# Optimization experiments

Measured on AMD Instinct MI355X. Metric: run time of the kernel, lower is better.

Reference implementation:

```python
import jax, jax.numpy as jnp
import numpy as np

NUM_HEADS = 8
H_NUM, W_NUM = 1, 2   # idx=0 stripe windows
SCALE = float((256 // NUM_HEADS) ** -0.5)  # qk_scale


def _partition(x, h_sp, w_sp):
    # x: (T,B,C,H,W) -> (T, B*nWin, heads, N, C//heads) with N = h_sp*w_sp
    T, B, C, H, W = x.shape
    x = x.reshape(T, B, C, H // h_sp, h_sp, W // w_sp, w_sp)
    x = x.transpose(0, 1, 3, 5, 4, 6, 2)  # T,B,nH,nW,h_sp,w_sp,C
    x = x.reshape(T, -1, h_sp * w_sp, NUM_HEADS, C // NUM_HEADS)
    return x.transpose(0, 1, 3, 2, 4)


def setup_inputs() -> dict:
    key = jax.random.key(0)
    k1, k2, k3 = jax.random.split(key, 3)
    shape = (4, 2, 256, 56, 56)
    return {
        "q": jax.random.normal(k1, shape, jnp.float32),
        "k": jax.random.normal(k2, shape, jnp.float32),
        "v": jax.random.normal(k3, shape, jnp.float32),
        "v_lamda": 1,
    }


def reference(q, k, v, v_lamda):
    T, B, C, H0, W0 = q.shape
    h_pad = (-H0) % H_NUM
    w_pad = (-W0) % W_NUM
    pad = ((0, 0), (0, 0), (0, 0), (0, h_pad), (0, w_pad))
    q = jnp.pad(q, pad)
    k = jnp.pad(k, pad)
    v = jnp.pad(v, pad)
    H, W = H0 + h_pad, W0 + w_pad
    h_sp, w_sp = H // H_NUM, W // W_NUM

    qw = _partition(q, h_sp, w_sp)  # (T, BnW, h, N, d)
    kw = _partition(k, h_sp, w_sp)
    vw = _partition(v, h_sp, w_sp)  # head dim = C*v_lamda//heads

    attn = jnp.einsum('twhnd,twhmd->twhnm', qw, kw)          # (QK^T), no softmax
    out = jnp.einsum('twhnm,twhmd->twhnd', attn, vw) * (SCALE * 2)

    # merge windows back: (T,BnW,h,N,d) -> (T,B,Cv,H,W)
    Cv = C * v_lamda
    out = out.transpose(0, 1, 3, 2, 4).reshape(T, -1, h_sp * w_sp, Cv)
    out = out.reshape(T, B, H_NUM, W_NUM, h_sp, w_sp, Cv)
    out = out.transpose(0, 1, 2, 4, 3, 5, 6).reshape(T, B, H, W, Cv)
    out = out.transpose(0, 1, 4, 2, 3)
    return out[:, :, :, :H0, :W0]
```

## Files before the change

kernel.cpp:

```cpp
#include <hip/hip_runtime.h>


#define HW 3136
#define WDIM 56
#define NPROB 128
#define SPLIT 14
#define PSPLIT 112
#define SCALE2 0.35355339059327373f

typedef const __attribute__((address_space(1))) void gas_void;
typedef __attribute__((address_space(3))) void las_void;
typedef float v2f __attribute__((ext_vector_type(2)));

__global__ __launch_bounds__(256) void kv_kernel(const float* __restrict__ K,
                                                 const float* __restrict__ V,
                                                 float* __restrict__ Mpart) {
    __shared__ float lds[2 * 32 * PSPLIT];

    const int blk = blockIdx.x;
    const int p   = blk / SPLIT;
    const int s   = blk - p * SPLIT;
    const int head = p & 7;
    const int win  = (p >> 3) & 1;
    const int b    = (p >> 4) & 1;
    const int t    = p >> 5;

    const size_t base = (size_t)((t * 2 + b) * 256 + head * 32) * HW;
    const float* __restrict__ Kb = K + base;
    const float* __restrict__ Vb = V + base;

    const int tid = threadIdx.x;
    const int l   = tid & 63;
    const int w   = tid >> 6;

    #pragma unroll
    for (int i = 0; i < 7; ++i) {
        const int q    = (w * 7 + i) * 64 + l;
        const int isv  = q >= 896 ? 1 : 0;
        const int r    = q - isv * 896;
        const int pq   = r >> 5;
        const int slot = r & 31;
        const int ch   = ((slot & 7) << 2) + (slot >> 3);
        const int n    = s * PSPLIT + pq * 4;
        const int y    = n / 28;
        const int x    = n - y * 28;
        const float* src = (isv ? Vb : Kb)
                         + (size_t)ch * HW + y * WDIM + win * 28 + x;
        float* dst = &lds[(w * 7 + i) * 256];
        __builtin_amdgcn_global_load_lds((gas_void*)src, (las_void*)dst, 16, 0, 0);
    }
    __syncthreads();

    const int g = l >> 3;
    const int e = l & 7;

    v2f acc2[4][4] = {};
    #pragma unroll
    for (int j = 0; j < 7; ++j) {
        const int rowb = (7 * w + j) * 128;
        float4 ka[4], va[4];
        #pragma unroll
        for (int i = 0; i < 4; ++i) {
            ka[i] = *(const float4*)&lds[rowb + (g + 8 * i) * 4];
            va[i] = *(const float4*)&lds[3584 + rowb + (e + 8 * i) * 4];
        }
        #pragma unroll
        for (int i = 0; i < 4; ++i) {
            const v2f ka_lo = {ka[i].x, ka[i].y};
            const v2f ka_hi = {ka[i].z, ka[i].w};
            #pragma unroll
            for (int jj = 0; jj < 4; ++jj) {
                const v2f va_lo = {va[jj].x, va[jj].y};
                const v2f va_hi = {va[jj].z, va[jj].w};
                acc2[i][jj] += ka_lo * va_lo;
                acc2[i][jj] += ka_hi * va_hi;
            }
        }
    }
    __syncthreads();

    const int dd0 = g * 4;
    const int de0 = e * 4;
    #pragma unroll
    for (int i = 0; i < 4; ++i)
        #pragma unroll
        for (int jj = 0; jj < 4; ++jj)
            lds[w * 1024 + (dd0 + i) * 32 + (de0 + jj)] = acc2[i][jj].x + acc2[i][jj].y;
    __syncthreads();

    const float4 r0 = *(const float4*)&lds[tid * 4];
    const float4 r1 = *(const float4*)&lds[1024 + tid * 4];
    const float4 r2 = *(const float4*)&lds[2048 + tid * 4];
    const float4 r3 = *(const float4*)&lds[3072 + tid * 4];
    float4 o;
    o.x = r0.x + r1.x + r2.x + r3.x;
    o.y = r0.y + r1.y + r2.y + r3.y;
    o.z = r0.z + r1.z + r2.z + r3.z;
    o.w = r0.w + r1.w + r2.w + r3.w;
    *(float4*)&Mpart[(size_t)blk * 1024 + tid * 4] = o;
}

__global__ __launch_bounds__(256) void qm_kernel(const float* __restrict__ Q,
                                                 const float* __restrict__ Mpart,
                                                 float* __restrict__ Out) {
    __shared__ float M[1024];
    const int blk = blockIdx.x;
    const int p   = blk / 7;
    const int c   = blk - p * 7;
    const int tid = threadIdx.x;

    const float* mp = Mpart + (size_t)p * SPLIT * 1024 + tid * 4;
    v2f s0 = {0.f, 0.f}, s1 = {0.f, 0.f};
    #pragma unroll
    for (int s = 0; s < SPLIT; ++s) {
        const float4 v = *(const float4*)&mp[s * 1024];
        const v2f vlo = {v.x, v.y};
        const v2f vhi = {v.z, v.w};
        s0 += vlo; s1 += vhi;
    }
    float4 sum;
    sum.x = s0.x * SCALE2; sum.y = s0.y * SCALE2;
    sum.z = s1.x * SCALE2; sum.w = s1.y * SCALE2;
    *(float4*)&M[tid * 4] = sum;
    __syncthreads();

    const int head = p & 7;
    const int win  = (p >> 3) & 1;
    const int b    = (p >> 4) & 1;
    const int t    = p >> 5;

    if (tid < 224) {
        const int n = c * 224 + tid;
        const int y = n / 28;
        const int x = n - y * 28;
        const size_t base = (size_t)((t * 2 + b) * 256 + head * 32) * HW
                          + y * WDIM + win * 28 + x;
        const float* __restrict__ Qb = Q + base;
        float* __restrict__ Ob = Out + base;

        float qv[32];
        #pragma unroll
        for (int dd = 0; dd < 32; ++dd)
            qv[dd] = Qb[(size_t)dd * HW];

        v2f acc2[16] = {};
        #pragma unroll 8
        for (int dd = 0; dd < 32; ++dd) {
            const v2f qq = {qv[dd], qv[dd]};
            #pragma unroll
            for (int gg = 0; gg < 8; ++gg) {
                const float4 m = *(const float4*)&M[dd * 32 + gg * 4];
                const v2f mlo = {m.x, m.y};
                const v2f mhi = {m.z, m.w};
                acc2[gg * 2 + 0] += qq * mlo;
                acc2[gg * 2 + 1] += qq * mhi;
            }
        }
        #pragma unroll
        for (int gg = 0; gg < 8; ++gg) {
            Ob[(size_t)(gg * 4 + 0) * HW] = acc2[gg * 2 + 0].x;
            Ob[(size_t)(gg * 4 + 1) * HW] = acc2[gg * 2 + 0].y;
            Ob[(size_t)(gg * 4 + 2) * HW] = acc2[gg * 2 + 1].x;
            Ob[(size_t)(gg * 4 + 3) * HW] = acc2[gg * 2 + 1].y;
        }
    }
}

extern "C" void kernel_launch(void* const* d_in, const int* in_sizes, int n_in,
                              void* d_out, int out_size, void* d_ws, size_t ws_size,
                              hipStream_t stream) {
    const float* q = (const float*)d_in[0];
    const float* k = (const float*)d_in[1];
    const float* v = (const float*)d_in[2];
    float* out   = (float*)d_out;
    float* Mpart = (float*)d_ws;

    kv_kernel<<<NPROB * SPLIT, 256, 0, stream>>>(k, v, Mpart);
    qm_kernel<<<NPROB * 7, 256, 0, stream>>>(q, Mpart, out);
}
```

Baseline: 129.2 us.

## Double-buffer KV reduction over fewer blocks and vectorize Q·M per-thread tiles

The KV kernel now runs 256 blocks that each loop over seven chunks with double-buffered global-to-LDS loads, explicit vmcnt waits and barriers, instead of 1792 single-chunk blocks. This cuts the partial-sum count from 14 to 2 per problem and lightens the Mpart reduction in the QM kernel. The QM kernel now gives each thread four pixels with float4 Q loads and float4 output stores, also over 256 blocks. The cost is much less parallelism: 256 blocks on a large GPU may leave CUs idle, and the wider accumulator set raises register pressure.

```diff
diff --git a/kernel.cpp b/kernel.cpp
--- a/kernel.cpp
+++ b/kernel.cpp
@@ -4,7 +4,6 @@
 #define HW 3136
 #define WDIM 56
 #define NPROB 128
-#define SPLIT 14
 #define PSPLIT 112
 #define SCALE2 0.35355339059327373f
 
@@ -15,11 +14,13 @@
 __global__ __launch_bounds__(256) void kv_kernel(const float* __restrict__ K,
                                                  const float* __restrict__ V,
                                                  float* __restrict__ Mpart) {
-    __shared__ float lds[2 * 32 * PSPLIT];
+    __shared__ float lds[2 * 7168];
+    float* bufA = lds;
+    float* bufB = lds + 7168;
 
-    const int blk = blockIdx.x;
-    const int p   = blk / SPLIT;
-    const int s   = blk - p * SPLIT;
+    const int g = blockIdx.x;
+    const int p = g >> 1;
+    const int h = g & 1;
     const int head = p & 7;
     const int win  = (p >> 3) & 1;
     const int b    = (p >> 4) & 1;
@@ -33,6 +34,7 @@
     const int l   = tid & 63;
     const int w   = tid >> 6;
 
+    const float* srcs[7];
     #pragma unroll
     for (int i = 0; i < 7; ++i) {
         const int q    = (w * 7 + i) * 64 + l;
@@ -41,45 +43,67 @@
         const int pq   = r >> 5;
         const int slot = r & 31;
         const int ch   = ((slot & 7) << 2) + (slot >> 3);
-        const int n    = s * PSPLIT + pq * 4;
+        const int n    = h * 7 * PSPLIT + pq * 4;
         const int y    = n / 28;
         const int x    = n - y * 28;
-        const float* src = (isv ? Vb : Kb)
-                         + (size_t)ch * HW + y * WDIM + win * 28 + x;
-        float* dst = &lds[(w * 7 + i) * 256];
-        __builtin_amdgcn_global_load_lds((gas_void*)src, (las_void*)dst, 16, 0, 0);
+        srcs[i] = (isv ? Vb : Kb) + (size_t)ch * HW + y * WDIM + win * 28 + x;
     }
-    __syncthreads();
 
-    const int g = l >> 3;
-    const int e = l & 7;
+    auto stage = [&](int c, float* buf) {
+        #pragma unroll
+        for (int i = 0; i < 7; ++i)
+            __builtin_amdgcn_global_load_lds((gas_void*)(srcs[i] + c * 224),
+                                             (las_void*)&buf[(w * 7 + i) * 256],
+                                             16, 0, 0);
+    };
 
+    const int gg = l >> 3;
+    const int e  = l & 7;
     v2f acc2[4][4] = {};
-    #pragma unroll
-    for (int j = 0; j < 7; ++j) {
-        const int rowb = (7 * w + j) * 128;
-        float4 ka[4], va[4];
+
+    auto compute = [&](const float* __restrict__ buf) {
         #pragma unroll
-        for (int i = 0; i < 4; ++i) {
-            ka[i] = *(const float4*)&lds[rowb + (g + 8 * i) * 4];
-            va[i] = *(const float4*)&lds[3584 + rowb + (e + 8 * i) * 4];
-        }
-        #pragma unroll
-        for (int i = 0; i < 4; ++i) {
-            const v2f ka_lo = {ka[i].x, ka[i].y};
-            const v2f ka_hi = {ka[i].z, ka[i].w};
+        for (int j = 0; j < 7; ++j) {
+            const int rowb = (7 * w + j) * 128;
+            float4 ka[4], va[4];
             #pragma unroll
-            for (int jj = 0; jj < 4; ++jj) {
-                const v2f va_lo = {va[jj].x, va[jj].y};
-                const v2f va_hi = {va[jj].z, va[jj].w};
-                acc2[i][jj] += ka_lo * va_lo;
-                acc2[i][jj] += ka_hi * va_hi;
+            for (int i = 0; i < 4; ++i) {
+                ka[i] = *(const float4*)&buf[rowb + (gg + 8 * i) * 4];
+                va[i] = *(const float4*)&buf[3584 + rowb + (e + 8 * i) * 4];
+            }
+            #pragma unroll
+            for (int i = 0; i < 4; ++i) {
+                const v2f ka_lo = {ka[i].x, ka[i].y};
+                const v2f ka_hi = {ka[i].z, ka[i].w};
+                #pragma unroll
+                for (int jj = 0; jj < 4; ++jj) {
+                    const v2f va_lo = {va[jj].x, va[jj].y};
+                    const v2f va_hi = {va[jj].z, va[jj].w};
+                    acc2[i][jj] += ka_lo * va_lo;
+                    acc2[i][jj] += ka_hi * va_hi;
+                }
             }
         }
+    };
+
+    stage(0, bufA);
+    stage(1, bufB);
+    #pragma unroll
+    for (int c = 0; c < 7; ++c) {
+        __builtin_amdgcn_sched_barrier(0);
+        if (c < 6) asm volatile("s_waitcnt vmcnt(7)" ::: "memory");
+        else       asm volatile("s_waitcnt vmcnt(0)" ::: "memory");
+        __builtin_amdgcn_sched_barrier(0);
+        __builtin_amdgcn_s_barrier();
+        __builtin_amdgcn_sched_barrier(0);
+        compute((c & 1) ? bufB : bufA);
+        __builtin_amdgcn_sched_barrier(0);
+        __builtin_amdgcn_s_barrier();
+        __builtin_amdgcn_sched_barrier(0);
+        if (c + 2 <= 6) stage(c + 2, (c & 1) ? bufB : bufA);
     }
-    __syncthreads();
 
-    const int dd0 = g * 4;
+    const int dd0 = gg * 4;
     const int de0 = e * 4;
     #pragma unroll
     for (int i = 0; i < 4; ++i)
@@ -97,30 +121,26 @@
     o.y = r0.y + r1.y + r2.y + r3.y;
     o.z = r0.z + r1.z + r2.z + r3.z;
     o.w = r0.w + r1.w + r2.w + r3.w;
-    *(float4*)&Mpart[(size_t)blk * 1024 + tid * 4] = o;
+    *(float4*)&Mpart[(size_t)g * 1024 + tid * 4] = o;
 }
 
 __global__ __launch_bounds__(256) void qm_kernel(const float* __restrict__ Q,
                                                  const float* __restrict__ Mpart,
                                                  float* __restrict__ Out) {
     __shared__ float M[1024];
-    const int blk = blockIdx.x;
-    const int p   = blk / 7;
-    const int c   = blk - p * 7;
+    const int g = blockIdx.x;
+    const int p = g >> 1;
+    const int h = g & 1;
     const int tid = threadIdx.x;
 
-    const float* mp = Mpart + (size_t)p * SPLIT * 1024 + tid * 4;
-    v2f s0 = {0.f, 0.f}, s1 = {0.f, 0.f};
-    #pragma unroll
-    for (int s = 0; s < SPLIT; ++s) {
-        const float4 v = *(const float4*)&mp[s * 1024];
-        const v2f vlo = {v.x, v.y};
-        const v2f vhi = {v.z, v.w};
-        s0 += vlo; s1 += vhi;
-    }
+    const float* mp = Mpart + (size_t)p * 2048 + tid * 4;
+    const float4 a0 = *(const float4*)mp;
+    const float4 a1 = *(const float4*)(mp + 1024);
     float4 sum;
-    sum.x = s0.x * SCALE2; sum.y = s0.y * SCALE2;
-    sum.z = s1.x * SCALE2; sum.w = s1.y * SCALE2;
+    sum.x = (a0.x + a1.x) * SCALE2;
+    sum.y = (a0.y + a1.y) * SCALE2;
+    sum.z = (a0.z + a1.z) * SCALE2;
+    sum.w = (a0.w + a1.w) * SCALE2;
     *(float4*)&M[tid * 4] = sum;
     __syncthreads();
 
@@ -129,39 +149,37 @@
     const int b    = (p >> 4) & 1;
     const int t    = p >> 5;
 
-    if (tid < 224) {
-        const int n = c * 224 + tid;
-        const int y = n / 28;
-        const int x = n - y * 28;
+    if (tid < 196) {
+        const int qd = h * 196 + tid;
+        const int y  = qd / 7;
+        const int x  = (qd - y * 7) * 4;
         const size_t base = (size_t)((t * 2 + b) * 256 + head * 32) * HW
                           + y * WDIM + win * 28 + x;
         const float* __restrict__ Qb = Q + base;
         float* __restrict__ Ob = Out + base;
 
-        float qv[32];
-        #pragma unroll
-        for (int dd = 0; dd < 32; ++dd)
-            qv[dd] = Qb[(size_t)dd * HW];
-
-        v2f acc2[16] = {};
+        v2f accL[32] = {};
+        v2f accH[32] = {};
         #pragma unroll 8
         for (int dd = 0; dd < 32; ++dd) {
-            const v2f qq = {qv[dd], qv[dd]};
+            const float4 q4 = *(const float4*)&Qb[(size_t)dd * HW];
+            const v2f qL = {q4.x, q4.y};
+            const v2f qH = {q4.z, q4.w};
             #pragma unroll
-            for (int gg = 0; gg < 8; ++gg) {
-                const float4 m = *(const float4*)&M[dd * 32 + gg * 4];
-                const v2f mlo = {m.x, m.y};
-                const v2f mhi = {m.z, m.w};
-                acc2[gg * 2 + 0] += qq * mlo;
-                acc2[gg * 2 + 1] += qq * mhi;
+            for (int de4 = 0; de4 < 8; ++de4) {
+                const float4 m = *(const float4*)&M[dd * 32 + de4 * 4];
+                accL[de4 * 4 + 0] += qL * m.x;  accH[de4 * 4 + 0] += qH * m.x;
+                accL[de4 * 4 + 1] += qL * m.y;  accH[de4 * 4 + 1] += qH * m.y;
+                accL[de4 * 4 + 2] += qL * m.z;  accH[de4 * 4 + 2] += qH * m.z;
+                accL[de4 * 4 + 3] += qL * m.w;  accH[de4 * 4 + 3] += qH * m.w;
             }
         }
         #pragma unroll
-        for (int gg = 0; gg < 8; ++gg) {
-            Ob[(size_t)(gg * 4 + 0) * HW] = acc2[gg * 2 + 0].x;
-            Ob[(size_t)(gg * 4 + 1) * HW] = acc2[gg * 2 + 0].y;
-            Ob[(size_t)(gg * 4 + 2) * HW] = acc2[gg * 2 + 1].x;
-            Ob[(size_t)(gg * 4 + 3) * HW] = acc2[gg * 2 + 1].y;
+        for (int de = 0; de < 32; ++de) {
+            float4 o;
+            o.x = accL[de].x; o.y = accL[de].y;
+            o.z = accH[de].x; o.w = accH[de].y;
+            *(float4*)&Ob[(size_t)de * HW] = o;
         }
     }
 }
@@ -175,6 +193,6 @@
     float* out   = (float*)d_out;
     float* Mpart = (float*)d_ws;
 
-    kv_kernel<<<NPROB * SPLIT, 256, 0, stream>>>(k, v, Mpart);
-    qm_kernel<<<NPROB * 7, 256, 0, stream>>>(q, Mpart, out);
+    kv_kernel<<<256, 256, 0, stream>>>(k, v, Mpart);
+    qm_kernel<<<256, 256, 0, stream>>>(q, Mpart, out);
 }
```

Measured after the change: 474.1 us. +266.9%, slower.
